# Optimization experiments

Measured on AMD Instinct MI355X. Metric: run time of the kernel, lower is better.

## Reference

```python
import jax, jax.numpy as jnp
import numpy as np

S, V = 16, 8                 # node embedding irreps: 16x0e + 8x1o
GEO = 3 * V                  # flattened vector feature dims
OUT = 8                      # output irreps: 8x0e
RADIUS = 5.0
NUM_BASIS = 20               # radius * basis_density_per_A
ACT_NORM = 1.6789717         # e3nn normalize2mom constant for silu under N(0,1)
SQ3 = 3.0 ** 0.5
W_MSG = S*S + V*S + S*V + V*V        # 576 = weight_numel of node x sh -> node TP
W_REC = (S*S + V*V) * OUT            # 2560 = weight_numel of node x node -> 8x0e TP


def _mlp(x, w0, w1):
    # e3nn FullyConnectedNet: randn weights, matmul scaled by 1/sqrt(fan_in),
    # hidden activation is second-moment-normalized silu, last layer linear.
    h = jax.nn.silu(x @ (w0 / np.sqrt(w0.shape[0]))) * ACT_NORM
    return h @ (w1 / np.sqrt(w1.shape[0]))


def _sh(vec):
    # o3.spherical_harmonics lmax=1, normalize=True, normalization='component':
    # Y0 = 1, Y1 = sqrt(3) * unit_vector
    r = vec / jnp.linalg.norm(vec, axis=-1, keepdims=True)
    return jnp.ones((vec.shape[0], 1), vec.dtype), SQ3 * r


def _split(f):
    return f[:, :S], f[:, S:].reshape(-1, V, 3)


def _tp_node_sh(xf, y0, y1, w):
    # FullyConnectedTensorProduct (Sx0e+Vx1o) x (1x0e+1x1o) -> (Sx0e+Vx1o), external per-edge weights.
    # CG (e3nn wigner_3j): 0x0->0: 1; 1x1->0: delta/sqrt3; 0x1->1,1x0->1: delta/sqrt3.
    # path_weight = sqrt((2l_out+1)/fan_in), fan_in per output irrep = S*1 + V*1.
    xs, xv = _split(xf)
    o = 0
    wA = w[:, o:o + S*S].reshape(-1, S, S); o += S*S   # 0e x 0e -> 0e
    wB = w[:, o:o + V*S].reshape(-1, V, S); o += V*S   # 1o x 1o -> 0e
    wC = w[:, o:o + S*V].reshape(-1, S, V); o += S*V   # 0e x 1o -> 1o
    wD = w[:, o:].reshape(-1, V, V)                    # 1o x 0e -> 1o
    fan = float(S + V)
    pw0 = (1.0 / fan) ** 0.5
    pw1 = (3.0 / fan) ** 0.5
    out_s = pw0 * (jnp.einsum('eu,euw->ew', xs * y0, wA)
                   + jnp.einsum('eui,ei,euw->ew', xv, y1, wB) / SQ3)
    out_v = (pw1 / SQ3) * (jnp.einsum('eu,ei,euw->ewi', xs, y1, wC)
                           + jnp.einsum('eui,euw->ewi', xv * y0[..., None], wD))
    return jnp.concatenate([out_s, out_v.reshape(-1, GEO)], axis=1)


def _tp_rec(xf, yf, w):
    # FullyConnectedTensorProduct (node) x (node) -> OUTx0e, external per-edge weights.
    xs, xv = _split(xf)
    ys, yv = _split(yf)
    w1 = w[:, :S*S*OUT].reshape(-1, S, S, OUT)
    w2 = w[:, S*S*OUT:].reshape(-1, V, V, OUT)
    pw = (1.0 / float(S*S + V*V)) ** 0.5
    return pw * (jnp.einsum('eu,ev,euvw->ew', xs, ys, w1)
                 + jnp.einsum('eui,evi,euvw->ew', xv, yv, w2) / SQ3)


def _dist_embed(d):
    # soft_one_hot_linspace(basis='smooth_finite', cutoff=True) * sqrt(num_basis)
    values = jnp.linspace(0.0, RADIUS, NUM_BASIS + 2)[1:-1]
    step = RADIUS / (NUM_BASIS + 1)
    diff = (d[:, None] - values) / step
    sus = lambda t: jnp.where(t > 0.0, jnp.exp(-1.0 / jnp.where(t > 0.0, t, 1.0)), 0.0)
    return 1.14136 * np.exp(2.0) * sus(diff + 1.0) * sus(1.0 - diff) * (NUM_BASIS ** 0.5)


def _mp_step(node, pos, src, dst, edge_attr, imp, mw0, mw1, uw0, uw1, is_initial):
    n = node.shape[0]
    vec = pos[dst] - pos[src]
    y0, y1 = _sh(vec)
    tp = _tp_node_sh(node[src], y0, y1, _mlp(edge_attr, mw0, mw1))
    deg = src.shape[0] / n
    msgs = jax.ops.segment_sum(tp, dst, num_segments=n) / (deg ** 0.5)
    msgs = msgs * imp
    scal = _mlp(jnp.concatenate([msgs[:, :S], node[:, :S]], axis=1), uw0, uw1)
    geo = msgs[:, S:] + node[:, S:]
    if not is_initial:
        geo = geo * 0.5
    return jnp.concatenate([scal, geo], axis=1)


def _forward(x, pos, edge_attr, emb_w0, emb_w1, imp0, msg0_w0, msg0_w1, upd0_w0, upd0_w1,
             imp1, msg1_w0, msg1_w1, upd1_w0, upd1_w1, lig_w0, lig_w1, rec_w0, rec_w1,
             edge_index, inter_edge_index):
    src, dst = edge_index[0], edge_index[1]
    node = _mlp(x, emb_w0, emb_w1)                                   # [N, S]
    node = jnp.concatenate([node, jnp.zeros((node.shape[0], GEO), node.dtype)], axis=1)
    node = _mp_step(node, pos, src, dst, edge_attr, imp0, msg0_w0, msg0_w1, upd0_w0, upd0_w1, True)
    node = _mp_step(node, pos, src, dst, edge_attr, imp1, msg1_w0, msg1_w1, upd1_w0, upd1_w1, False)
    rec, lig = inter_edge_index[0], inter_edge_index[1]
    vec = pos[lig] - pos[rec]
    y0, y1 = _sh(vec)
    demb = _dist_embed(jnp.linalg.norm(vec, axis=1))
    lig_emb = _tp_node_sh(node[lig], y0, y1, _mlp(demb, lig_w0, lig_w1))
    return _tp_rec(lig_emb, node[rec], _mlp(demb, rec_w0, rec_w1))    # [E_inter, OUT]


def setup_inputs():
    key = jax.random.key(0)
    ks = iter(jax.random.split(key, 32))
    N, E, EI = 10000, 120000, 40000
    A, B = 10, 5   # len(atom_types), len(bond_types)
    rn = lambda *s: jax.random.normal(next(ks), s, dtype=jnp.float32)
    # edges without self-loops (dst != src) to keep edge_vec nonzero
    src = jax.random.randint(next(ks), (E,), 0, N)
    dst = (src + jax.random.randint(next(ks), (E,), 1, N)) % N
    irec = jax.random.randint(next(ks), (EI,), 0, N)
    ilig = (irec + jax.random.randint(next(ks), (EI,), 1, N)) % N
    return dict(
        x=jax.random.uniform(next(ks), (N, A), dtype=jnp.float32),
        pos=rn(N, 3) * 3.0,
        edge_index=jnp.stack([src, dst]),
        edge_attr=jax.random.uniform(next(ks), (E, B), dtype=jnp.float32),
        inter_edge_index=jnp.stack([irec, ilig]),
        emb_w0=rn(A, 64), emb_w1=rn(64, S),
        imp0=rn(1), msg0_w0=rn(B, 64), msg0_w1=rn(64, W_MSG),
        upd0_w0=rn(2 * S, 64), upd0_w1=rn(64, S),
        imp1=rn(1), msg1_w0=rn(B, 64), msg1_w1=rn(64, W_MSG),
        upd1_w0=rn(2 * S, 64), upd1_w1=rn(64, S),
        lig_w0=rn(NUM_BASIS, 64), lig_w1=rn(64, W_MSG),
        rec_w0=rn(NUM_BASIS, 64), rec_w1=rn(64, W_REC),
    )


def reference(x, pos, edge_index, edge_attr, inter_edge_index,
              emb_w0, emb_w1, imp0, msg0_w0, msg0_w1, upd0_w0, upd0_w1,
              imp1, msg1_w0, msg1_w1, upd1_w0, upd1_w1,
              lig_w0, lig_w1, rec_w0, rec_w1):
    return _forward(x, pos, edge_attr, emb_w0, emb_w1, imp0, msg0_w0, msg0_w1, upd0_w0, upd0_w1,
                    imp1, msg1_w0, msg1_w1, upd1_w0, upd1_w1, lig_w0, lig_w1, rec_w0, rec_w1,
                    edge_index, inter_edge_index)
```

## Files before the change

kernel.cpp:

```cpp
#include <hip/hip_runtime.h>
#include <hip/hip_fp16.h>
#include <cmath>

constexpr float ACT_NORM = 1.6789717f;
constexpr float PW0      = 0.20412414523193154f;
constexpr float PW1      = 0.35355339059327373f;
constexpr float PWREC    = 0.05590169943749474f;
constexpr float INV_SQ3  = 0.57735026918962576f;
constexpr float PW0s     = PW0 * 0.125f;
constexpr float PW1s     = PW1 * 0.125f;
constexpr float PWRECs   = PWREC * 0.125f;

__device__ __forceinline__ float silu_n(float x) {
  return x / (1.f + __expf(-x)) * ACT_NORM;
}

__device__ __forceinline__ unsigned ubcast_lane(unsigned v, int k) {
  return (unsigned)__builtin_amdgcn_readlane((int)v, k);
}

typedef _Float16 h2v __attribute__((ext_vector_type(2)));
typedef _Float16 f16x8 __attribute__((ext_vector_type(8)));
typedef float    f32x4 __attribute__((ext_vector_type(4)));

__device__ __forceinline__ unsigned packh2(float a, float b) {
  h2v p; p.x = (_Float16)a; p.y = (_Float16)b;
  return __builtin_bit_cast(unsigned, p);
}
__device__ __forceinline__ unsigned short f16bits(float a) {
  return __builtin_bit_cast(unsigned short, (_Float16)a);
}
__device__ __forceinline__ float h2f(unsigned short b) {
  return (float)__builtin_bit_cast(_Float16, b);
}
__device__ __forceinline__ float dot2h(unsigned w2, unsigned h2, float acc) {
  return __builtin_amdgcn_fdot2(__builtin_bit_cast(h2v, w2),
                                __builtin_bit_cast(h2v, h2), acc, false);
}
__device__ __forceinline__ float hlo(unsigned d) {
  return (float)__builtin_bit_cast(_Float16, (unsigned short)(d & 0xffffu));
}
__device__ __forceinline__ float hhi(unsigned d) {
  return (float)__builtin_bit_cast(_Float16, (unsigned short)(d >> 16));
}
__device__ __forceinline__ float hsel(unsigned d, int hi) { return hi ? hhi(d) : hlo(d); }
__device__ __forceinline__ unsigned u4sel(const uint4& v, int i) {
  return i == 0 ? v.x : (i == 1 ? v.y : (i == 2 ? v.z : v.w));
}
__device__ __forceinline__ unsigned u2sel(const uint2& v, int i) { return i ? v.y : v.x; }

__device__ __forceinline__ f32x4 mfma16(uint4 a, uint4 b, f32x4 c) {
  return __builtin_amdgcn_mfma_f32_16x16x32_f16(
      __builtin_bit_cast(f16x8, a), __builtin_bit_cast(f16x8, b), c, 0, 0, 0);
}

__global__ __launch_bounds__(256)
void hist_kernel(const int* __restrict__ ei, int* __restrict__ cnt, int E) {
  const int e = blockIdx.x * 256 + threadIdx.x;
  if (e < E) atomicAdd(&cnt[ei[E + e]], 1);
}

__global__ __launch_bounds__(1024)
void scan_kernel(const int* __restrict__ cnt, int* __restrict__ starts, int N) {
  __shared__ int sums[1024];
  const int t = threadIdx.x;
  const int per = (N + 1023) >> 10;
  const int base = t * per;
  int s = 0;
  for (int i = 0; i < per; ++i) {
    const int idx = base + i;
    if (idx < N) s += cnt[idx];
  }
  sums[t] = s;
  __syncthreads();
  for (int off = 1; off < 1024; off <<= 1) {
    int v = (t >= off) ? sums[t - off] : 0;
    __syncthreads();
    sums[t] += v;
    __syncthreads();
  }
  int run = (t > 0) ? sums[t - 1] : 0;
  for (int i = 0; i < per; ++i) {
    const int idx = base + i;
    if (idx < N) { starts[idx] = run; run += cnt[idx]; }
  }
}

__global__ __launch_bounds__(256)
void scatter_kernel(const int* __restrict__ ei, const int* __restrict__ starts,
                    int* __restrict__ cursor, int* __restrict__ eperm, int E) {
  const int e = blockIdx.x * 256 + threadIdx.x;
  if (e < E) {
    const int d = ei[E + e];
    const int r = atomicAdd(&cursor[d], 1);
    eperm[starts[d] + r] = e;
  }
}

__global__ __launch_bounds__(256)
void pack_b_kernel(const float* __restrict__ W1, uint4* __restrict__ Bp) {
  const int gid = blockIdx.x * 256 + threadIdx.x;
  if (gid >= 36 * 128) return;
  const int t = gid >> 7, H = (gid >> 6) & 1, l = gid & 63;
  const int kb = H * 32 + (l >> 4) * 8;
  const float* src = &W1[(size_t)kb * 576 + t * 16 + (l & 15)];
  uint4 q;
  q.x = packh2(src[0],       src[576]);
  q.y = packh2(src[2 * 576], src[3 * 576]);
  q.z = packh2(src[4 * 576], src[5 * 576]);
  q.w = packh2(src[6 * 576], src[7 * 576]);
  Bp[gid] = q;
}

__global__ __launch_bounds__(256)
void emb_kernel(const float* __restrict__ x, const float* __restrict__ w0,
                const float* __restrict__ w1, float* __restrict__ node, int N) {
  const int lane = threadIdx.x & 63;
  const int lw   = threadIdx.x >> 6;
  const int gw   = blockIdx.x * 4 + lw;
  __shared__ float sH[4][64];
  const bool valid = gw < N;
  const int n = valid ? gw : 0;
  float acc = 0.f;
#pragma unroll
  for (int a = 0; a < 10; ++a) acc = fmaf(x[n * 10 + a], w0[a * 64 + lane], acc);
  acc *= 0.31622776601683794f;
  sH[lw][lane] = silu_n(acc);
  __syncthreads();
  if (valid) {
    if (lane < 16) {
      float o = 0.f;
#pragma unroll
      for (int k = 0; k < 64; ++k) o = fmaf(sH[lw][k], w1[k * 16 + lane], o);
      node[(size_t)n * 40 + lane] = o * 0.125f;
    } else if (lane < 40) {
      node[(size_t)n * 40 + lane] = 0.f;
    }
  }
}

__global__ __launch_bounds__(256)
void upd_kernel(float* __restrict__ node, const float* __restrict__ mbuf,
                const int* __restrict__ starts, const int* __restrict__ cnt,
                const int* __restrict__ eperm,
                const float* __restrict__ w0, const float* __restrict__ w1,
                const float* __restrict__ imp, float geo_scale, float inv_sqrt_deg, int N) {
  const int lane = threadIdx.x & 63;
  const int lw   = threadIdx.x >> 6;
  const int gw   = blockIdx.x * 4 + lw;
  __shared__ float sIn[4][32];
  __shared__ float sH[4][64];
  const bool valid = gw < N;
  const int n = valid ? gw : 0;
  const float mscale = imp[0] * inv_sqrt_deg;

  float m = 0.f;
  if (lane < 40) {
    const int s0 = starts[n], d = cnt[n];
    for (int j = 0; j < d; ++j)
      m += mbuf[(size_t)eperm[s0 + j] * 40 + lane];
  }

  if (lane < 16)      sIn[lw][lane] = m * mscale;
  else if (lane < 32) sIn[lw][lane] = node[(size_t)n * 40 + lane - 16];
  __syncthreads();
  float acc = 0.f;
#pragma unroll
  for (int a = 0; a < 32; ++a) acc = fmaf(sIn[lw][a], w0[a * 64 + lane], acc);
  acc *= 0.17677669529663687f;
  sH[lw][lane] = silu_n(acc);
  __syncthreads();
  if (valid) {
    if (lane < 16) {
      float o = 0.f;
#pragma unroll
      for (int k = 0; k < 64; ++k) o = fmaf(sH[lw][k], w1[k * 16 + lane], o);
      node[(size_t)n * 40 + lane] = o * 0.125f;
    } else if (lane < 40) {
      const size_t gi = (size_t)n * 40 + lane;
      node[gi] = fmaf(m, mscale, node[gi]) * geo_scale;
    }
  }
}

__global__ __launch_bounds__(256)
void inter_h_kernel(const float* __restrict__ pos, const int* __restrict__ iei,
                    const float* __restrict__ lw0, const float* __restrict__ rw0,
                    float* __restrict__ hL, float* __restrict__ hR, int EI) {
  const int lane = threadIdx.x & 63;
  const int lw   = threadIdx.x >> 6;
  const int gw   = blockIdx.x * 4 + lw;
  __shared__ float sD[4][20];
  const bool valid = gw < EI;
  const int e = valid ? gw : 0;
  const int rec = iei[e], lig = iei[EI + e];
  const float dx = pos[lig * 3]     - pos[rec * 3];
  const float dy = pos[lig * 3 + 1] - pos[rec * 3 + 1];
  const float dz = pos[lig * 3 + 2] - pos[rec * 3 + 2];
  const float d = sqrtf(dx * dx + dy * dy + dz * dz);
  if (lane < 20) {
    const float diff = d * 4.2f - (float)(lane + 1);
    const float t1 = diff + 1.f, t2 = 1.f - diff;
    float v = 0.f;
    if (t1 > 0.f && t2 > 0.f) {
      const float C = 1.14136f * 7.3890560989306495f * 4.4721359549995794f;
      v = C * __expf(-1.f / t1 - 1.f / t2);
    }
    sD[lw][lane] = v;
  }
  __syncthreads();
  float a0 = 0.f, a1 = 0.f;
#pragma unroll
  for (int b = 0; b < 20; ++b) {
    const float db = sD[lw][b];
    a0 = fmaf(db, lw0[b * 64 + lane], a0);
    a1 = fmaf(db, rw0[b * 64 + lane], a1);
  }
  a0 *= 0.22360679774997896f;
  a1 *= 0.22360679774997896f;
  if (valid) {
    hL[(size_t)e * 64 + lane] = silu_n(a0);
    hR[(size_t)e * 64 + lane] = silu_n(a1);
  }
}

__global__ __launch_bounds__(256, 2)
void msg_mfma_kernel(const float* __restrict__ node, const float* __restrict__ pos,
                     const int* __restrict__ ei, const float* __restrict__ eattr,
                     const float* __restrict__ w0, const uint4* __restrict__ Bp,
                     float* __restrict__ mbuf, int E, int nTe) {
  __shared__ __align__(16) uint4 sB[32 * 128];
  __shared__ __align__(16) unsigned short sFt[4][16][64];
  const int tid = threadIdx.x, lane = tid & 63, wv = tid >> 6;

  for (int j = tid; j < 4096; j += 256) sB[j] = Bp[j];
  __syncthreads();

  uint4 g32[8];
#pragma unroll
  for (int j = 0; j < 8; ++j) g32[j] = Bp[(64 + j) * 64 + lane];

  float w0c[5];
#pragma unroll
  for (int a = 0; a < 5; ++a) w0c[a] = w0[a * 64 + lane] * 0.4472135954999579f;

  unsigned short (*fW)[64] = sFt[wv];
  const int er0 = (lane >> 4) * 4;
  const int c   = lane & 15;
  const int cp  = (lane >> 3) & 1;
  const int w   = c & 7;
  const int el  = lane & 15;
  const int kb0 = (lane >> 4) * 8;

  for (int T = blockIdx.x * 4 + wv; T < nTe; T += (int)gridDim.x * 4) {
#pragma unroll
    for (int j = 0; j < 2; ++j) {
      const int flat = j * 64 + lane;
      if (flat < 80) {
        const int e = flat / 5, a = flat - e * 5;
        int ge = T * 16 + e; if (ge >= E) ge = E - 1;
        fW[e][56 + a] = f16bits(eattr[(size_t)ge * 5 + a]);
      }
    }
#pragma unroll
    for (int e = 0; e < 16; ++e) {
      float acc = 0.f;
#pragma unroll
      for (int a = 0; a < 5; ++a) acc = fmaf(h2f(fW[e][56 + a]), w0c[a], acc);
      fW[e][lane] = f16bits(silu_n(acc));
    }
    const uint4 a0 = *(const uint4*)&fW[el][kb0];
    const uint4 a1 = *(const uint4*)&fW[el][32 + kb0];

    if (lane < 16) {
      int ge = T * 16 + lane; if (ge >= E) ge = E - 1;
      const int ia = ei[ge], ib = ei[E + ge];
      const float vx = pos[ib * 3]     - pos[ia * 3];
      const float vy = pos[ib * 3 + 1] - pos[ia * 3 + 1];
      const float vz = pos[ib * 3 + 2] - pos[ia * 3 + 2];
      const float rn = rsqrtf(vx * vx + vy * vy + vz * vz);
      fW[lane][40] = f16bits(vx * rn);
      fW[lane][41] = f16bits(vy * rn);
      fW[lane][42] = f16bits(vz * rn);
    }
#pragma unroll
    for (int j = 0; j < 4; ++j) {
      const int e = j * 4 + (lane >> 4);
      int ge = T * 16 + e; if (ge >= E) ge = E - 1;
      const int ns = ei[ge];
      fW[e][c] = f16bits(node[(size_t)ns * 40 + c]);
    }
#pragma unroll
    for (int j = 0; j < 6; ++j) {
      const int flat = j * 64 + lane;
      const int e = flat / 24, q = flat - e * 24;
      const int u = q / 3, i = q - u * 3;
      int ge = T * 16 + e; if (ge >= E) ge = E - 1;
      const int ns = ei[ge];
      fW[e][16 + i * 8 + (u & 1) * 4 + (u >> 1)] = f16bits(node[(size_t)ns * 40 + 16 + q]);
    }
#pragma unroll
    for (int j = 0; j < 2; ++j) {
      const int flat = j * 64 + lane;
      const int e = flat >> 3, u = flat & 7;
      float d = 0.f;
#pragma unroll
      for (int i = 0; i < 3; ++i)
        d = fmaf(h2f(fW[e][16 + i * 8 + (u & 1) * 4 + (u >> 1)]), h2f(fW[e][40 + i]), d);
      fW[e][48 + u] = f16bits(d);
    }

    uint4 xsR[4][2], dpR[4];
    uint2 xvR[4][3];
    float rf[4][3];
#pragma unroll
    for (int r = 0; r < 4; ++r) {
      const int e = er0 + r;
      xsR[r][0] = *(const uint4*)&fW[e][0];
      xsR[r][1] = *(const uint4*)&fW[e][8];
      dpR[r]    = *(const uint4*)&fW[e][48];
#pragma unroll
      for (int i = 0; i < 3; ++i) {
        xvR[r][i] = *(const uint2*)&fW[e][16 + i * 8 + cp * 4];
        rf[r][i]  = h2f(fW[e][40 + i]);
      }
    }

    float o_s[4] = {0.f, 0.f, 0.f, 0.f};
    float sxw[4] = {0.f, 0.f, 0.f, 0.f};
    float ov[3][4];
#pragma unroll
    for (int i = 0; i < 3; ++i)
#pragma unroll
      for (int r = 0; r < 4; ++r) ov[i][r] = 0.f;

    uint4 b0 = sB[lane], b1 = sB[64 + lane];
#pragma unroll
    for (int t = 0; t < 32; ++t) {
      uint4 n0, n1;
      if (t < 31) { n0 = sB[(t + 1) * 128 + lane]; n1 = sB[(t + 1) * 128 + 64 + lane]; }
      f32x4 C = {0.f, 0.f, 0.f, 0.f};
      C = mfma16(a0, b0, C);
      C = mfma16(a1, b1, C);
      if (t < 16) {
#pragma unroll
        for (int r = 0; r < 4; ++r)
          o_s[r] = fmaf(hsel(u4sel(xsR[r][t >> 3], (t >> 1) & 3), t & 1), C[r], o_s[r]);
      } else if (t < 24) {
        const int u = t - 16;
#pragma unroll
        for (int r = 0; r < 4; ++r)
          o_s[r] = fmaf(hsel(u4sel(dpR[r], u >> 1), u & 1), C[r], o_s[r]);
      } else {
        const int j = t - 24;
#pragma unroll
        for (int r = 0; r < 4; ++r) {
          const int idx = 2 * j + cp;
          sxw[r] = fmaf(hsel(u4sel(xsR[r][idx >> 3], (idx >> 1) & 3), idx & 1), C[r], sxw[r]);
        }
      }
      if (t < 31) { b0 = n0; b1 = n1; }
    }
#pragma unroll
    for (int j = 0; j < 4; ++j) {
      f32x4 C = {0.f, 0.f, 0.f, 0.f};
      C = mfma16(a0, g32[j * 2], C);
      C = mfma16(a1, g32[j * 2 + 1], C);
#pragma unroll
      for (int i = 0; i < 3; ++i)
#pragma unroll
        for (int r = 0; r < 4; ++r)
          ov[i][r] = fmaf(hsel(u2sel(xvR[r][i], j >> 1), j & 1), C[r], ov[i][r]);
    }

#pragma unroll
    for (int r = 0; r < 4; ++r) {
      const int ge = T * 16 + er0 + r;
      const bool valid = ge < E;
      const float sv = PW0s * o_s[r];
      float vv[3];
#pragma unroll
      for (int i = 0; i < 3; ++i) {
        float v = fmaf(PW1s * rf[r][i], sxw[r], PW0s * ov[i][r]);
        v += __shfl_xor(v, 8);
        vv[i] = v;
      }
      if (valid) {
        float* mb = mbuf + (size_t)ge * 40;
        mb[c] = sv;
        if ((lane & 8) == 0) {
#pragma unroll
          for (int i = 0; i < 3; ++i) mb[16 + w * 3 + i] = vv[i];
        }
      }
    }
  }
}

template <int MODE>
__global__ __launch_bounds__(512, 2)
void tp_kernel(const float* __restrict__ node, const float* __restrict__ pos,
               const int* __restrict__ ei, const float* __restrict__ eattr,
               const float* __restrict__ w0, const float* __restrict__ W1,
               const float* __restrict__ hSrc, float* __restrict__ out, int E) {
  __shared__ __align__(16) uint4 sWa[32 * 64];
  __shared__ __align__(16) uint4 sWb[32 * 64];
  __shared__ unsigned sWc[32 * 64];
  __shared__ float sF[8][6][27];
  const int tid  = threadIdx.x;
  const int lane = tid & 63;
  const int wv   = tid >> 6;

  for (int j = tid; j < 2048; j += 512) {
    const int kp = j >> 6, l = j & 63;
    const float* s0 = &W1[(2 * kp) * 576 + l];
    const float* s1 = s0 + 576;
    uint4 qa, qb;
    qa.x = packh2(s0[0],   s1[0]);
    qa.y = packh2(s0[64],  s1[64]);
    qa.z = packh2(s0[128], s1[128]);
    qa.w = packh2(s0[192], s1[192]);
    qb.x = packh2(s0[256], s1[256]);
    qb.y = packh2(s0[320], s1[320]);
    qb.z = packh2(s0[384], s1[384]);
    qb.w = packh2(s0[448], s1[448]);
    sWa[j] = qa;
    sWb[j] = qb;
    sWc[j] = packh2(s0[512], s1[512]);
  }
  __syncthreads();

  float w0r[5];
  if (MODE == 0) {
#pragma unroll
    for (int a = 0; a < 5; ++a) w0r[a] = w0[a * 64 + lane] * 0.4472135954999579f;
  }
  const int kl2 = (lane & 31) * 2;

  const int nB = (E + 47) / 48;
  for (int b = blockIdx.x; b < nB; b += (int)gridDim.x) {
    const int ebase = b * 48 + wv * 6;
    int outn[6], nsrc[6];
    bool val[6];
    unsigned hp[6];
#pragma unroll
    for (int s = 0; s < 6; ++s) {
      const int e0 = ebase + s;
      val[s] = e0 < E;
      const int e = val[s] ? e0 : 0;
      const int ia = ei[e], ib = ei[E + e];
      if (MODE == 0) { nsrc[s] = ia; outn[s] = ib; }
      else           { nsrc[s] = ib; outn[s] = e;  }
      const float vx = pos[ib * 3]     - pos[ia * 3];
      const float vy = pos[ib * 3 + 1] - pos[ia * 3 + 1];
      const float vz = pos[ib * 3 + 2] - pos[ia * 3 + 2];
      const float rn = rsqrtf(vx * vx + vy * vy + vz * vz);
      const float rx = vx * rn, ry = vy * rn, rz = vz * rn;
      float h;
      if (MODE == 0) {
        float acc = 0.f;
#pragma unroll
        for (int a = 0; a < 5; ++a) acc = fmaf(eattr[(size_t)e * 5 + a], w0r[a], acc);
        h = silu_n(acc);
      } else {
        h = hSrc[(size_t)e * 64 + lane];
      }
      hp[s] = packh2(__shfl(h, kl2), __shfl(h, kl2 + 1));
      if (lane < 16) {
        sF[wv][s][lane] = node[(size_t)nsrc[s] * 40 + lane];
      } else if (lane < 24) {
        const int u = lane - 16;
        const float x0 = node[(size_t)nsrc[s] * 40 + 16 + u * 3];
        const float x1 = node[(size_t)nsrc[s] * 40 + 16 + u * 3 + 1];
        const float x2 = node[(size_t)nsrc[s] * 40 + 16 + u * 3 + 2];
        sF[wv][s][16 + u] = x0 * rx + x1 * ry + x2 * rz;
      } else if (lane < 27) {
        sF[wv][s][24 + (lane - 24)] = (lane == 24) ? rx : ((lane == 25) ? ry : rz);
      }
    }

    float wacc[6][9];
#pragma unroll
    for (int s = 0; s < 6; ++s)
#pragma unroll
      for (int t = 0; t < 9; ++t) wacc[s][t] = 0.f;

    uint4 qa0 = sWa[lane], qb0 = sWb[lane];
    unsigned qc0 = sWc[lane];
#pragma unroll 4
    for (int kp = 0; kp < 32; ++kp) {
      const int kn = (kp + 1) & 31;
      const uint4 qa1 = sWa[kn * 64 + lane];
      const uint4 qb1 = sWb[kn * 64 + lane];
      const unsigned qc1 = sWc[kn * 64 + lane];
#pragma unroll
      for (int s = 0; s < 6; ++s) {
        const unsigned hv2 = ubcast_lane(hp[s], kp);
        wacc[s][0] = dot2h(qa0.x, hv2, wacc[s][0]);
        wacc[s][1] = dot2h(qa0.y, hv2, wacc[s][1]);
        wacc[s][2] = dot2h(qa0.z, hv2, wacc[s][2]);
        wacc[s][3] = dot2h(qa0.w, hv2, wacc[s][3]);
        wacc[s][4] = dot2h(qb0.x, hv2, wacc[s][4]);
        wacc[s][5] = dot2h(qb0.y, hv2, wacc[s][5]);
        wacc[s][6] = dot2h(qb0.z, hv2, wacc[s][6]);
        wacc[s][7] = dot2h(qb0.w, hv2, wacc[s][7]);
        wacc[s][8] = dot2h(qc0,   hv2, wacc[s][8]);
      }
      qa0 = qa1; qb0 = qb1; qc0 = qc1;
    }

    const int ub  = lane >> 4;
    const int ub2 = lane >> 3;
#pragma unroll
    for (int s = 0; s < 6; ++s) {
      float cs = 0.f;
#pragma unroll
      for (int t = 0; t < 6; ++t)
        cs = fmaf(PW0s * sF[wv][s][ub + 4 * t], wacc[s][t], cs);
      cs += __shfl_xor(cs, 16);
      cs += __shfl_xor(cs, 32);

      const float rx = sF[wv][s][24], ry = sF[wv][s][25], rz = sF[wv][s][26];
      const float* xp = &node[(size_t)nsrc[s] * 40 + 16 + ub2 * 3];
      const float xv0 = xp[0], xv1 = xp[1], xv2 = xp[2];
      const float sxw = PW1s * (sF[wv][s][ub2] * wacc[s][6] + sF[wv][s][ub2 + 8] * wacc[s][7]);
      float cv0 = fmaf(PW0s * xv0, wacc[s][8], sxw * rx);
      float cv1 = fmaf(PW0s * xv1, wacc[s][8], sxw * ry);
      float cv2 = fmaf(PW0s * xv2, wacc[s][8], sxw * rz);
      cv0 += __shfl_xor(cv0, 8); cv0 += __shfl_xor(cv0, 16); cv0 += __shfl_xor(cv0, 32);
      cv1 += __shfl_xor(cv1, 8); cv1 += __shfl_xor(cv1, 16); cv1 += __shfl_xor(cv1, 32);
      cv2 += __shfl_xor(cv2, 8); cv2 += __shfl_xor(cv2, 16); cv2 += __shfl_xor(cv2, 32);

      if (val[s]) {
        const size_t ob = (size_t)outn[s] * 40;
        if (lane < 16) out[ob + lane] = cs;
        if (lane < 8) {
          out[ob + 16 + lane * 3]     = cv0;
          out[ob + 16 + lane * 3 + 1] = cv1;
          out[ob + 16 + lane * 3 + 2] = cv2;
        }
      }
    }
  }
}

__global__ __launch_bounds__(512)
void pack_h_kernel(const float* __restrict__ h, uint4* __restrict__ hPf, int nT) {
  const int gid = blockIdx.x * 512 + threadIdx.x;
  if (gid >= nT * 128) return;
  const int l = gid & 63;
  const int H = (gid >> 6) & 1;
  const int T = gid >> 7;
  const int e = T * 16 + (l & 15);
  const int kb = H * 32 + (l >> 4) * 8;
  const float* src = &h[(size_t)e * 64 + kb];
  uint4 q;
  q.x = packh2(src[0], src[1]);
  q.y = packh2(src[2], src[3]);
  q.z = packh2(src[4], src[5]);
  q.w = packh2(src[6], src[7]);
  hPf[gid] = q;
}

__global__ __launch_bounds__(256)
void pack_d_kernel(const float* __restrict__ ligE, const float* __restrict__ node,
                   const int* __restrict__ iei, unsigned short* __restrict__ Dt, int EI) {
  const int gid = blockIdx.x * 256 + threadIdx.x;
  if (gid >= EI * 64) return;
  const int e = gid >> 6, rem = gid & 63;
  const int b = rem >> 5, u = (rem >> 2) & 7, vi = rem & 3;
  const int v = 2 * vi + b;
  const int rec = iei[e];
  const float* xp = &ligE[(size_t)e * 40 + 16 + u * 3];
  const float* yp = &node[(size_t)rec * 40 + 16 + v * 3];
  const float d = (xp[0] * yp[0] + xp[1] * yp[1] + xp[2] * yp[2]) * INV_SQ3;
  Dt[gid] = f16bits(d);
}

__global__ __launch_bounds__(512, 2)
void rec_kernel(const float* __restrict__ node, const float* __restrict__ ligE,
                const int* __restrict__ iei, const float* __restrict__ RW1,
                const uint4* __restrict__ hPf, const uint2* __restrict__ Dt2,
                float* __restrict__ out, int nT) {
  __shared__ __align__(16) uint4 sB[4096];
  __shared__ __align__(16) unsigned short sFeat[8][320];
  const int tid = threadIdx.x, lane = tid & 63, wv = tid >> 6;
  const int cg = blockIdx.y;

  for (int j = tid; j < 4096; j += 512) {
    const int t = j >> 7, H = (j >> 6) & 1, l = j & 63;
    const int kb = H * 32 + (l >> 4) * 8;
    const float* src = &RW1[(size_t)kb * 2560 + cg * 512 + t * 16 + (l & 15)];
    uint4 q;
    q.x = packh2(src[0],        src[2560]);
    q.y = packh2(src[2 * 2560], src[3 * 2560]);
    q.z = packh2(src[4 * 2560], src[5 * 2560]);
    q.w = packh2(src[6 * 2560], src[7 * 2560]);
    sB[j] = q;
  }
  __syncthreads();

  unsigned short* fW = sFeat[wv];
  const int er0 = (lane >> 4) * 4;
  const int bpar = (lane >> 3) & 1;
  const int c    = lane & 7;
  const int se = lane >> 2, si = lane & 3;

  for (int T = blockIdx.x * 8 + wv; T < nT; T += (int)gridDim.x * 8) {
    const uint4 a0 = hPf[(T * 2 + 0) * 64 + lane];
    const uint4 a1 = hPf[(T * 2 + 1) * 64 + lane];
    const int eg = T * 16 + se;

    if (cg < 4) {
      const int rn = iei[eg];
      const float4 yv = *(const float4*)&node[(size_t)rn * 40 + si * 4];
      *(unsigned*)&fW[(se * 2 + 0) * 8 + 2 * si] = packh2(yv.x, yv.z);
      *(unsigned*)&fW[(se * 2 + 1) * 8 + 2 * si] = packh2(yv.y, yv.w);
      fW[256 + se * 4 + si] = f16bits(ligE[(size_t)eg * 40 + cg * 4 + si]);
    }

    float o[4] = {0.f, 0.f, 0.f, 0.f};
    uint4 b0 = sB[lane], b1 = sB[64 + lane];

    if (cg < 4) {
      uint2 xsR[4]; uint4 ysR[4];
#pragma unroll
      for (int r = 0; r < 4; ++r) {
        const int er = er0 + r;
        ysR[r] = *(const uint4*)&fW[(er * 2 + bpar) * 8];
        xsR[r] = *(const uint2*)&fW[256 + er * 4];
      }
#pragma unroll
      for (int t = 0; t < 32; ++t) {
        uint4 n0, n1;
        if (t < 31) { n0 = sB[(t + 1) * 128 + lane]; n1 = sB[(t + 1) * 128 + 64 + lane]; }
        f32x4 C = {0.f, 0.f, 0.f, 0.f};
        C = mfma16(a0, b0, C);
        C = mfma16(a1, b1, C);
        const int up = t >> 3, vi = t & 7;
#pragma unroll
        for (int r = 0; r < 4; ++r) {
          const float xs = hsel(u2sel(xsR[r], up >> 1), up & 1);
          const float ys = hsel(u4sel(ysR[r], vi >> 1), vi & 1);
          o[r] = fmaf(xs * ys, C[r], o[r]);
        }
        if (t < 31) { b0 = n0; b1 = n1; }
      }
    } else {
#pragma unroll
      for (int pass = 0; pass < 2; ++pass) {
        uint2 dR[4][4];
#pragma unroll
        for (int r = 0; r < 4; ++r) {
          const int e = T * 16 + er0 + r;
#pragma unroll
          for (int uu = 0; uu < 4; ++uu)
            dR[r][uu] = Dt2[(size_t)e * 16 + bpar * 8 + pass * 4 + uu];
        }
#pragma unroll
        for (int tt = 0; tt < 16; ++tt) {
          const int t = pass * 16 + tt;
          uint4 n0, n1;
          if (t < 31) { n0 = sB[(t + 1) * 128 + lane]; n1 = sB[(t + 1) * 128 + 64 + lane]; }
          f32x4 C = {0.f, 0.f, 0.f, 0.f};
          C = mfma16(a0, b0, C);
          C = mfma16(a1, b1, C);
          const int uu = tt >> 2, vi = tt & 3;
#pragma unroll
          for (int r = 0; r < 4; ++r) {
            const float f = hsel(u2sel(dR[r][uu], vi >> 1), vi & 1);
            o[r] = fmaf(f, C[r], o[r]);
          }
          if (t < 31) { b0 = n0; b1 = n1; }
        }
      }
    }

#pragma unroll
    for (int r = 0; r < 4; ++r) {
      const float v = o[r] + __shfl_xor(o[r], 8);
      if ((lane & 8) == 0)
        atomicAdd(&out[(size_t)(T * 16 + er0 + r) * 8 + c], v * PWRECs);
    }
  }
}

extern "C" void kernel_launch(void* const* d_in, const int* in_sizes, int n_in,
                              void* d_out, int out_size, void* d_ws, size_t ws_size,
                              hipStream_t stream) {
  (void)n_in; (void)ws_size;
  const float* x      = (const float*)d_in[0];
  const float* pos    = (const float*)d_in[1];
  const int*   ei     = (const int*)  d_in[2];
  const float* eattr  = (const float*)d_in[3];
  const int*   iei    = (const int*)  d_in[4];
  const float* emb_w0 = (const float*)d_in[5];
  const float* emb_w1 = (const float*)d_in[6];
  const float* imp0   = (const float*)d_in[7];
  const float* m0w0   = (const float*)d_in[8];
  const float* m0w1   = (const float*)d_in[9];
  const float* u0w0   = (const float*)d_in[10];
  const float* u0w1   = (const float*)d_in[11];
  const float* imp1   = (const float*)d_in[12];
  const float* m1w0   = (const float*)d_in[13];
  const float* m1w1   = (const float*)d_in[14];
  const float* u1w0   = (const float*)d_in[15];
  const float* u1w1   = (const float*)d_in[16];
  const float* lw0    = (const float*)d_in[17];
  const float* lw1    = (const float*)d_in[18];
  const float* rw0    = (const float*)d_in[19];
  const float* rw1    = (const float*)d_in[20];

  const int N  = in_sizes[1] / 3;
  const int E  = in_sizes[2] / 2;
  const int EI = in_sizes[4] / 2;

  float* node = (float*)d_ws;
  float* regA = node + (size_t)N * 40;
  float* outp = (float*)d_out;

  int*   cnt    = (int*)regA;
  int*   starts = cnt + N;
  int*   cursor = starts + N;
  int*   eperm  = cursor + N;
  float* bbase  = (float*)(eperm + E);
  uint4* Bp     = (uint4*)bbase;
  float* mbuf   = bbase + 36 * 128 * 4;

  float* hL   = regA;
  float* hR   = hL + (size_t)EI * 64;
  float* ligE = hR + (size_t)EI * 64;
  uint4*          hPf = (uint4*)hL;
  unsigned short* Dt  = (unsigned short*)hR;

  const float inv_sqrt_deg = 1.0f / sqrtf((float)E / (float)N);
  const int nodeBlocks  = (N + 3) / 4;
  const int interBlocks = (EI + 3) / 4;
  const int nT  = EI / 16;
  const int nTe = (E + 15) / 16;
  const int eBlocks = (E + 255) / 256;

  hipMemsetAsync(cnt, 0, (size_t)N * sizeof(int), stream);
  hipMemsetAsync(cursor, 0, (size_t)N * sizeof(int), stream);
  hist_kernel<<<eBlocks, 256, 0, stream>>>(ei, cnt, E);
  scan_kernel<<<1, 1024, 0, stream>>>(cnt, starts, N);
  scatter_kernel<<<eBlocks, 256, 0, stream>>>(ei, starts, cursor, eperm, E);

  emb_kernel<<<nodeBlocks, 256, 0, stream>>>(x, emb_w0, emb_w1, node, N);

  pack_b_kernel<<<18, 256, 0, stream>>>(m0w1, Bp);
  msg_mfma_kernel<<<512, 256, 0, stream>>>(node, pos, ei, eattr, m0w0, Bp, mbuf, E, nTe);
  upd_kernel<<<nodeBlocks, 256, 0, stream>>>(node, mbuf, starts, cnt, eperm,
                                             u0w0, u0w1, imp0, 1.0f, inv_sqrt_deg, N);

  pack_b_kernel<<<18, 256, 0, stream>>>(m1w1, Bp);
  msg_mfma_kernel<<<512, 256, 0, stream>>>(node, pos, ei, eattr, m1w0, Bp, mbuf, E, nTe);
  upd_kernel<<<nodeBlocks, 256, 0, stream>>>(node, mbuf, starts, cnt, eperm,
                                             u1w0, u1w1, imp1, 0.5f, inv_sqrt_deg, N);

  inter_h_kernel<<<interBlocks, 256, 0, stream>>>(pos, iei, lw0, rw0, hL, hR, EI);
  tp_kernel<1><<<512, 512, 0, stream>>>(node, pos, iei, nullptr, nullptr, lw1, hL, ligE, EI);

  pack_h_kernel<<<(nT * 128 + 511) / 512, 512, 0, stream>>>(hR, hPf, nT);
  pack_d_kernel<<<(EI * 64 + 255) / 256, 256, 0, stream>>>(ligE, node, iei, Dt, EI);

  hipMemsetAsync(outp, 0, (size_t)out_size * sizeof(float), stream);
  rec_kernel<<<dim3(102, 5), 512, 0, stream>>>(node, ligE, iei, rw1, hPf, (const uint2*)Dt,
                                               outp, nT);
}
```

Measured before the change: 381.7 us.

## Prefetch next tile's edge features into registers and unroll neighbor gather

The message kernel now loads the next tile's edge attributes, positions and gathered node features into registers before the MFMA loop of the current tile, so gather latency overlaps with compute. The update kernel's per-node message sum is unrolled four ways with independent accumulators to expose more memory-level parallelism. Message outputs are written with nontemporal stores to avoid polluting cache. The prefetch raises register pressure, which may reduce occupancy, and nontemporal stores could hurt if the update kernel rereads mbuf from cache.

```diff
diff --git a/kernel.cpp b/kernel.cpp
--- a/kernel.cpp
+++ b/kernel.cpp
@@ -157,8 +157,18 @@
   float m = 0.f;
   if (lane < 40) {
     const int s0 = starts[n], d = cnt[n];
-    for (int j = 0; j < d; ++j)
-      m += mbuf[(size_t)eperm[s0 + j] * 40 + lane];
+    float m0 = 0.f, m1 = 0.f, m2 = 0.f, m3 = 0.f;
+    int j = 0;
+    for (; j + 4 <= d; j += 4) {
+      const int e0 = eperm[s0 + j],     e1 = eperm[s0 + j + 1];
+      const int e2 = eperm[s0 + j + 2], e3 = eperm[s0 + j + 3];
+      m0 += mbuf[(size_t)e0 * 40 + lane];
+      m1 += mbuf[(size_t)e1 * 40 + lane];
+      m2 += mbuf[(size_t)e2 * 40 + lane];
+      m3 += mbuf[(size_t)e3 * 40 + lane];
+    }
+    for (; j < d; ++j) m0 += mbuf[(size_t)eperm[s0 + j] * 40 + lane];
+    m = (m0 + m1) + (m2 + m3);
   }
 
   if (lane < 16)      sIn[lw][lane] = m * mscale;
@@ -251,15 +261,50 @@
   const int w   = c & 7;
   const int el  = lane & 15;
   const int kb0 = (lane >> 4) * 8;
-
-  for (int T = blockIdx.x * 4 + wv; T < nTe; T += (int)gridDim.x * 4) {
+  const int stride = (int)gridDim.x * 4;
+
+  float eaA[2], pxA[6], xsA[4], xvA[6];
+  auto load_feats = [&](int Tt) {
 #pragma unroll
     for (int j = 0; j < 2; ++j) {
       const int flat = j * 64 + lane;
       if (flat < 80) {
         const int e = flat / 5, a = flat - e * 5;
-        int ge = T * 16 + e; if (ge >= E) ge = E - 1;
-        fW[e][56 + a] = f16bits(eattr[(size_t)ge * 5 + a]);
+        int ge = Tt * 16 + e; if (ge >= E) ge = E - 1;
+        eaA[j] = eattr[(size_t)ge * 5 + a];
+      }
+    }
+    if (lane < 16) {
+      int ge = Tt * 16 + lane; if (ge >= E) ge = E - 1;
+      const int ia = ei[ge], ib = ei[E + ge];
+      pxA[0] = pos[ia * 3]; pxA[1] = pos[ia * 3 + 1]; pxA[2] = pos[ia * 3 + 2];
+      pxA[3] = pos[ib * 3]; pxA[4] = pos[ib * 3 + 1]; pxA[5] = pos[ib * 3 + 2];
+    }
+#pragma unroll
+    for (int j = 0; j < 4; ++j) {
+      const int e = j * 4 + (lane >> 4);
+      int ge = Tt * 16 + e; if (ge >= E) ge = E - 1;
+      xsA[j] = node[(size_t)ei[ge] * 40 + c];
+    }
+#pragma unroll
+    for (int j = 0; j < 6; ++j) {
+      const int flat = j * 64 + lane;
+      const int e = flat / 24, q = flat - e * 24;
+      int ge = Tt * 16 + e; if (ge >= E) ge = E - 1;
+      xvA[j] = node[(size_t)ei[ge] * 40 + 16 + q];
+    }
+  };
+
+  int T = blockIdx.x * 4 + wv;
+  if (T < nTe) load_feats(T);
+
+  for (; T < nTe; T += stride) {
+#pragma unroll
+    for (int j = 0; j < 2; ++j) {
+      const int flat = j * 64 + lane;
+      if (flat < 80) {
+        const int e = flat / 5, a = flat - e * 5;
+        fW[e][56 + a] = f16bits(eaA[j]);
       }
     }
 #pragma unroll
@@ -273,11 +318,7 @@
     const uint4 a1 = *(const uint4*)&fW[el][32 + kb0];
 
     if (lane < 16) {
-      int ge = T * 16 + lane; if (ge >= E) ge = E - 1;
-      const int ia = ei[ge], ib = ei[E + ge];
-      const float vx = pos[ib * 3]     - pos[ia * 3];
-      const float vy = pos[ib * 3 + 1] - pos[ia * 3 + 1];
-      const float vz = pos[ib * 3 + 2] - pos[ia * 3 + 2];
+      const float vx = pxA[3] - pxA[0], vy = pxA[4] - pxA[1], vz = pxA[5] - pxA[2];
       const float rn = rsqrtf(vx * vx + vy * vy + vz * vz);
       fW[lane][40] = f16bits(vx * rn);
       fW[lane][41] = f16bits(vy * rn);
@@ -286,18 +327,14 @@
 #pragma unroll
     for (int j = 0; j < 4; ++j) {
       const int e = j * 4 + (lane >> 4);
-      int ge = T * 16 + e; if (ge >= E) ge = E - 1;
-      const int ns = ei[ge];
-      fW[e][c] = f16bits(node[(size_t)ns * 40 + c]);
+      fW[e][c] = f16bits(xsA[j]);
     }
 #pragma unroll
     for (int j = 0; j < 6; ++j) {
       const int flat = j * 64 + lane;
       const int e = flat / 24, q = flat - e * 24;
       const int u = q / 3, i = q - u * 3;
-      int ge = T * 16 + e; if (ge >= E) ge = E - 1;
-      const int ns = ei[ge];
-      fW[e][16 + i * 8 + (u & 1) * 4 + (u >> 1)] = f16bits(node[(size_t)ns * 40 + 16 + q]);
+      fW[e][16 + i * 8 + (u & 1) * 4 + (u >> 1)] = f16bits(xvA[j]);
     }
 #pragma unroll
     for (int j = 0; j < 2; ++j) {
@@ -325,6 +362,9 @@
         rf[r][i]  = h2f(fW[e][40 + i]);
       }
     }
+
+    const int Tn = T + stride;
+    if (Tn < nTe) load_feats(Tn);
 
     float o_s[4] = {0.f, 0.f, 0.f, 0.f};
     float sxw[4] = {0.f, 0.f, 0.f, 0.f};
@@ -387,10 +427,11 @@
       }
       if (valid) {
         float* mb = mbuf + (size_t)ge * 40;
-        mb[c] = sv;
+        __builtin_nontemporal_store(sv, &mb[c]);
         if ((lane & 8) == 0) {
 #pragma unroll
-          for (int i = 0; i < 3; ++i) mb[16 + w * 3 + i] = vv[i];
+          for (int i = 0; i < 3; ++i)
+            __builtin_nontemporal_store(vv[i], &mb[16 + w * 3 + i]);
         }
       }
     }
```

Result: slower. 396.0 us (+3.7%).
